# Kernel optimization log

Measured on AMD Instinct MI355X. Metric: run time of the kernel, lower is better.

The kernel has to match this reference:

```python
import jax, jax.numpy as jnp
import numpy as np

HIDDEN = 1024
BATCH = 8192
N_STEPS = 50


def setup_inputs() -> dict:
    key = jax.random.key(0)
    k1, k2, k3 = jax.random.split(key, 3)
    x0 = jax.random.normal(k1, (HIDDEN, BATCH), dtype=jnp.float32)
    W = jax.random.normal(k2, (HIDDEN, HIDDEN), dtype=jnp.float32) * (1.0 / np.sqrt(HIDDEN))
    b = jax.random.normal(k3, (HIDDEN, 1), dtype=jnp.float32)
    t0 = jnp.zeros((), dtype=jnp.float32)
    t1 = jnp.ones((), dtype=jnp.float32)
    return {"x0": x0, "t0": t0, "t1": t1, "W": W, "b": b}


def reference(x0, t0, t1, W, b):
    # Euler integration: x_{i+1} = x_i + h * (W @ x_i + b), h = (t1 - t0) / N
    h = (t1 - t0) / N_STEPS

    def step(x, _):
        x = x + h * (W @ x + b)  # b [H,1] broadcasts over batch
        return x, None

    x_final, _ = jax.lax.scan(step, x0, None, length=N_STEPS)
    return x_final
```

## Files before the change

### kernel.cpp

```cpp
#include <hip/hip_runtime.h>

#define H 1024
#define HH (H * H)
#define BATCH 8192
#define NSTEPS 50

typedef __attribute__((ext_vector_type(8))) short bf16x8;
typedef __attribute__((ext_vector_type(4))) float f32x4;

__device__ __forceinline__ void split2(float a, unsigned short& h, unsigned short& l)
{
    unsigned u = __float_as_uint(a);
    float r = a - __uint_as_float(u & 0xFFFF0000u);
    h = (unsigned short)(u >> 16);
    l = (unsigned short)((__float_as_uint(r) + 0x8000u) >> 16);
}
__device__ __forceinline__ unsigned short rnd_bf16(float a)
{
    return (unsigned short)((__float_as_uint(a) + 0x8000u) >> 16);
}
__device__ __forceinline__ float bf2f(unsigned short s)
{
    return __uint_as_float(((unsigned)s) << 16);
}
__device__ __forceinline__ void gload16(const void* g, void* l)
{
    __builtin_amdgcn_global_load_lds(
        (const __attribute__((address_space(1))) void*)g,
        (__attribute__((address_space(3))) void*)l, 16, 0, 0);
}
#define VMCNT(n) asm volatile("s_waitcnt vmcnt(" #n ")" ::: "memory")
#define RBAR() do { __builtin_amdgcn_s_barrier(); __builtin_amdgcn_sched_barrier(0); } while (0)

__global__ void setup_k(const float* __restrict__ W, const float* __restrict__ bvec,
                        const float* __restrict__ t0, const float* __restrict__ t1,
                        unsigned short* __restrict__ Aplanes,
                        float* __restrict__ cv, float* __restrict__ v0)
{
    __shared__ unsigned short th[64][68], tl[64][68];
    const float h = (t1[0] - t0[0]) / (float)NSTEPS;
    const int bid = blockIdx.x, tid = threadIdx.x;
    const int rb = (bid >> 4) * 64, cb = (bid & 15) * 64;
    const int row = tid >> 2, c16 = (tid & 3) * 16;

    unsigned short* Ahi  = Aplanes;
    unsigned short* Alo  = Aplanes + HH;
    unsigned short* AhiT = Aplanes + 2 * HH;
    unsigned short* AloT = Aplanes + 3 * HH;

    {
        const float* wsrc = &W[(size_t)(rb + row) * H + cb + c16];
        bf16x8 hv[2], lv[2];
        #pragma unroll
        for (int q = 0; q < 16; ++q) {
            const float a = h * wsrc[q] + ((rb + row) == (cb + c16 + q) ? 1.0f : 0.0f);
            unsigned short hh, ll;
            split2(a, hh, ll);
            hv[q >> 3][q & 7] = (short)hh;
            lv[q >> 3][q & 7] = (short)ll;
            th[row][c16 + q] = hh;
            tl[row][c16 + q] = ll;
        }
        *(bf16x8*)&Ahi[(size_t)(rb + row) * H + cb + c16] = hv[0];
        *(bf16x8*)&Ahi[(size_t)(rb + row) * H + cb + c16 + 8] = hv[1];
        *(bf16x8*)&Alo[(size_t)(rb + row) * H + cb + c16] = lv[0];
        *(bf16x8*)&Alo[(size_t)(rb + row) * H + cb + c16 + 8] = lv[1];
    }
    __syncthreads();
    {
        bf16x8 hv[2], lv[2];
        #pragma unroll
        for (int q = 0; q < 16; ++q) {
            hv[q >> 3][q & 7] = (short)th[c16 + q][row];
            lv[q >> 3][q & 7] = (short)tl[c16 + q][row];
        }
        *(bf16x8*)&AhiT[(size_t)(cb + row) * H + rb + c16] = hv[0];
        *(bf16x8*)&AhiT[(size_t)(cb + row) * H + rb + c16 + 8] = hv[1];
        *(bf16x8*)&AloT[(size_t)(cb + row) * H + rb + c16] = lv[0];
        *(bf16x8*)&AloT[(size_t)(cb + row) * H + rb + c16 + 8] = lv[1];
    }
    if (bid == 0) {
        #pragma unroll
        for (int rep = 0; rep < 4; ++rep) {
            const int i = tid + rep * 256;
            const float v = h * bvec[i];
            cv[i] = v; v0[i] = v;
        }
    }
}

template<bool WRITE_T, bool DO_X>
__launch_bounds__(512)
__global__ void chain_fused_k(const unsigned short* __restrict__ Lhi,
                              const unsigned short* __restrict__ Llo,
                              const unsigned short* __restrict__ RThi,
                              const unsigned short* __restrict__ RTlo,
                              unsigned short* __restrict__ Qhi,
                              unsigned short* __restrict__ Qlo,
                              unsigned short* __restrict__ QhiT,
                              unsigned short* __restrict__ QloT,
                              const float* __restrict__ vin,
                              const float* __restrict__ addv,
                              float* __restrict__ vout,
                              const float* __restrict__ X,
                              unsigned short* __restrict__ XhiT)
{
    __shared__ unsigned short sA[2][2][2][64][32];
    __shared__ unsigned short sB[2][2][2][64][32];

    const int tid = threadIdx.x;
    const int bid = blockIdx.x;
    const int wave = tid >> 6, lane = tid & 63;

    if (DO_X && bid >= 272) {
        float (*ts)[65] = (float(*)[65])&sA[0][0][0][0][0];
        const int tile = bid - 272;
        const int n0x = (tile >> 4) * 64, k0x = (tile & 15) * 64;
        #pragma unroll
        for (int p = 0; p < 2; ++p) {
            const int kr = p * 32 + (tid >> 4);
            const int c4 = (tid & 15) * 4;
            const float4 v = *(const float4*)&X[(size_t)(k0x + kr) * BATCH + n0x + c4];
            ts[kr][c4 + 0] = v.x; ts[kr][c4 + 1] = v.y;
            ts[kr][c4 + 2] = v.z; ts[kr][c4 + 3] = v.w;
        }
        __syncthreads();
        {
            const int n = tid >> 3;
            const int kc = (tid & 7) * 8;
            bf16x8 hv;
            #pragma unroll
            for (int q = 0; q < 8; ++q)
                hv[q] = (short)rnd_bf16(ts[kc + q][n]);
            *(bf16x8*)&XhiT[(size_t)(n0x + n) * H + k0x + kc] = hv;
        }
        return;
    }

    if (bid >= 256) {
        const int rowbase = (bid - 256) * 64 + wave * 8;
        const float4* xq = (const float4*)vin + lane * 4;
        float4 xv[4];
        #pragma unroll
        for (int q = 0; q < 4; ++q) xv[q] = xq[q];
        #pragma unroll
        for (int rr = 0; rr < 8; ++rr) {
            const int row = rowbase + rr;
            const unsigned short* mh = Lhi + (size_t)row * H + lane * 16;
            const unsigned short* ml = Llo + (size_t)row * H + lane * 16;
            bf16x8 h0 = *(const bf16x8*)&mh[0];
            bf16x8 h1 = *(const bf16x8*)&mh[8];
            bf16x8 l0 = *(const bf16x8*)&ml[0];
            bf16x8 l1 = *(const bf16x8*)&ml[8];
            float s = 0.0f;
            #pragma unroll
            for (int q = 0; q < 8; ++q) {
                const float m0v = bf2f((unsigned short)h0[q]) + bf2f((unsigned short)l0[q]);
                const float m1v = bf2f((unsigned short)h1[q]) + bf2f((unsigned short)l1[q]);
                const float* xf = (const float*)xv;
                s = fmaf(m0v, xf[q], s);
                s = fmaf(m1v, xf[8 + q], s);
            }
            #pragma unroll
            for (int off = 32; off; off >>= 1)
                s += __shfl_down(s, off, 64);
            if (lane == 0) vout[row] = addv[row] + s;
        }
        return;
    }

    const int lg = lane >> 4, lm = lane & 15;
    const int half = wave >> 2;
    const int wq = wave & 3;
    const int wr2 = (wq >> 1) * 32, wc2 = (wq & 1) * 32;
    const int xcd = bid & 7;
    const int idx0 = bid >> 3;
    const int mt = (xcd >> 1) * 4 + (idx0 & 3);
    const int nt = (xcd & 1) * 8 + (idx0 >> 2);
    const int m0 = mt * 64, n0 = nt * 64;

    f32x4 acc[2][2] = {};

    #define CSTAGE(tt, b) do {                                                   \
        _Pragma("unroll")                                                        \
        for (int it = 0; it < 4; ++it) {                                         \
            const int idx = tid + it * 512;                                      \
            const int mat = idx >> 10, kh = (idx >> 9) & 1;                      \
            const int plane = (idx >> 8) & 1;                                    \
            const int row = (idx >> 2) & 63, kc = idx & 3;                       \
            const int ks = kc ^ ((row >> 1) & 3);                                \
            const unsigned short* g = mat ? (plane ? RTlo : RThi)                \
                                          : (plane ? Llo : Lhi);                 \
            const int rb = mat ? n0 : m0;                                        \
            unsigned short* d = mat ? &sB[b][kh][plane][row][kc * 8]             \
                                    : &sA[b][kh][plane][row][kc * 8];            \
            gload16(g + (size_t)(rb + row) * H + kh * 512 + (tt) * 32 + ks * 8, d); \
        }                                                                        \
    } while (0)

    CSTAGE(0, 0);
    __syncthreads();
    int buf = 0;
    for (int t = 0; t < 16; ++t) {
        if (t + 1 < 16) CSTAGE(t + 1, buf ^ 1);
        bf16x8 ah[2], al[2], bh[2], bl[2];
        #pragma unroll
        for (int i = 0; i < 2; ++i) {
            const int row = wr2 + i * 16 + lm;
            const int sl = lg ^ ((row >> 1) & 3);
            ah[i] = *(const bf16x8*)&sA[buf][half][0][row][sl * 8];
            al[i] = *(const bf16x8*)&sA[buf][half][1][row][sl * 8];
            const int rn = wc2 + i * 16 + lm;
            const int sn = lg ^ ((rn >> 1) & 3);
            bh[i] = *(const bf16x8*)&sB[buf][half][0][rn][sn * 8];
            bl[i] = *(const bf16x8*)&sB[buf][half][1][rn][sn * 8];
        }
        #pragma unroll
        for (int i = 0; i < 2; ++i)
            #pragma unroll
            for (int j = 0; j < 2; ++j) {
                acc[i][j] = __builtin_amdgcn_mfma_f32_16x16x32_bf16(ah[i], bh[j], acc[i][j], 0, 0, 0);
                acc[i][j] = __builtin_amdgcn_mfma_f32_16x16x32_bf16(ah[i], bl[j], acc[i][j], 0, 0, 0);
                acc[i][j] = __builtin_amdgcn_mfma_f32_16x16x32_bf16(al[i], bh[j], acc[i][j], 0, 0, 0);
            }
        __syncthreads();
        buf ^= 1;
    }
    #undef CSTAGE

    float* red = (float*)&sA[0][0][0][0][0];
    const int ridx = wq * 64 + lane;
    if (half == 1) {
        float* dst = red + (size_t)ridx * 17;
        #pragma unroll
        for (int i = 0; i < 2; ++i)
            #pragma unroll
            for (int j = 0; j < 2; ++j)
                *(f32x4*)&dst[(i * 2 + j) * 4] = acc[i][j];
    }
    __syncthreads();
    if (half == 0) {
        const float* src = red + (size_t)ridx * 17;
        #pragma unroll
        for (int i = 0; i < 2; ++i)
            #pragma unroll
            for (int j = 0; j < 2; ++j) {
                const f32x4 p = *(const f32x4*)&src[(i * 2 + j) * 4];
                acc[i][j] += p;
            }
        #pragma unroll
        for (int i = 0; i < 2; ++i) {
            const int row0 = m0 + wr2 + i * 16 + lg * 4;
            #pragma unroll
            for (int j = 0; j < 2; ++j) {
                const int col = n0 + wc2 + j * 16 + lm;
                unsigned short hs[4], ls[4];
                #pragma unroll
                for (int r = 0; r < 4; ++r) {
                    split2(acc[i][j][r], hs[r], ls[r]);
                    Qhi[(size_t)(row0 + r) * H + col] = hs[r];
                    Qlo[(size_t)(row0 + r) * H + col] = ls[r];
                }
                if (WRITE_T) {
                    ushort4 th, tl;
                    th.x = hs[0]; th.y = hs[1]; th.z = hs[2]; th.w = hs[3];
                    tl.x = ls[0]; tl.y = ls[1]; tl.z = ls[2]; tl.w = ls[3];
                    *(ushort4*)&QhiT[(size_t)col * H + row0] = th;
                    *(ushort4*)&QloT[(size_t)col * H + row0] = tl;
                }
            }
        }
    }
}

__launch_bounds__(512)
__global__ void big_gemm_pipe_k(const unsigned short* __restrict__ Phi,
                                const unsigned short* __restrict__ Plo,
                                const unsigned short* __restrict__ XhiT,
                                float* __restrict__ C, const float* __restrict__ bias)
{
    __shared__ unsigned short sA[3][2][128][32];
    __shared__ unsigned short sB[3][256][32];

    const int tid = threadIdx.x;
    const int wave = tid >> 6, lane = tid & 63;
    const int lg = lane >> 4, lm = lane & 15;
    const int wr2 = (wave >> 2) * 64;
    const int wc2 = (wave & 3) * 64;
    const int bid = blockIdx.x;
    const int l = bid >> 3;
    const int m0 = (l & 7) * 128;
    const int n0 = ((bid & 7) * 4 + (l >> 3)) * 256;

    f32x4 acc[4][4] = {};

    #define BSTAGE(tt, b) do {                                                     \
        const int r_ = tid >> 2, kc_ = tid & 3;                                    \
        const int ks_ = kc_ ^ ((r_ >> 1) & 3);                                     \
        const size_t go_ = (size_t)(tt) * 32 + ks_ * 8;                            \
        gload16(Phi  + (size_t)(m0 + r_) * H + go_, &sA[b][0][r_][kc_ * 8]);       \
        gload16(Plo  + (size_t)(m0 + r_) * H + go_, &sA[b][1][r_][kc_ * 8]);       \
        gload16(XhiT + (size_t)(n0 + r_) * H + go_, &sB[b][r_][kc_ * 8]);          \
        gload16(XhiT + (size_t)(n0 + 128 + r_) * H + go_, &sB[b][128 + r_][kc_ * 8]); \
    } while (0)

    BSTAGE(0, 0);
    BSTAGE(1, 1);
    VMCNT(4);
    RBAR();

    #pragma unroll
    for (int t = 0; t < 32; ++t) {
        const int b = t % 3;
        bf16x8 ah[4], al[4], bh[4];
        #pragma unroll
        for (int i = 0; i < 4; ++i) {
            const int row = wr2 + i * 16 + lm;
            const int sl = lg ^ ((row >> 1) & 3);
            ah[i] = *(const bf16x8*)&sA[b][0][row][sl * 8];
            al[i] = *(const bf16x8*)&sA[b][1][row][sl * 8];
        }
        #pragma unroll
        for (int j = 0; j < 4; ++j) {
            const int rn = wc2 + j * 16 + lm;
            const int sn = lg ^ ((rn >> 1) & 3);
            bh[j] = *(const bf16x8*)&sB[b][rn][sn * 8];
        }
        if (t + 2 < 32) BSTAGE(t + 2, (t + 2) % 3);
        __builtin_amdgcn_s_setprio(1);
        #pragma unroll
        for (int i = 0; i < 4; ++i)
            #pragma unroll
            for (int j = 0; j < 4; ++j) {
                acc[i][j] = __builtin_amdgcn_mfma_f32_16x16x32_bf16(ah[i], bh[j], acc[i][j], 0, 0, 0);
                acc[i][j] = __builtin_amdgcn_mfma_f32_16x16x32_bf16(al[i], bh[j], acc[i][j], 0, 0, 0);
            }
        __builtin_amdgcn_s_setprio(0);
        if (t < 30) VMCNT(4);
        else if (t == 30) VMCNT(0);
        if (t < 31) RBAR();
    }
    #undef BSTAGE

    #pragma unroll
    for (int i = 0; i < 4; ++i) {
        const int row0 = m0 + wr2 + i * 16 + lg * 4;
        #pragma unroll
        for (int r = 0; r < 4; ++r) {
            const float bv = bias[row0 + r];
            float* dst = &C[(size_t)(row0 + r) * BATCH + n0 + wc2 + lm];
            #pragma unroll
            for (int j = 0; j < 4; ++j)
                dst[j * 16] = acc[i][j][r] + bv;
        }
    }
}

#define PADK 40

__launch_bounds__(256)
__global__ void big_gemm_k(const unsigned short* __restrict__ Ahi_g,
                           const unsigned short* __restrict__ Alo_g,
                           const float* __restrict__ X, float* __restrict__ C,
                           const float* __restrict__ bias)
{
    __shared__ unsigned short Ahi[128][PADK], Alo[128][PADK];
    __shared__ unsigned short Bhi[128][PADK], Blo[128][PADK];

    const int tid = threadIdx.x;
    const int wave = tid >> 6;
    const int lane = tid & 63;
    const int wr = (wave >> 1) * 64;
    const int wc = (wave & 1) * 64;
    const int m0 = blockIdx.y * 128;
    const int n0 = blockIdx.x * 128;
    const int lg = lane >> 4;
    const int lm = lane & 15;

    f32x4 acc[4][4] = {};

    for (int k0 = 0; k0 < H; k0 += 32) {
        #pragma unroll
        for (int a2 = 0; a2 < 2; ++a2) {
            const int id = tid + a2 * 256;
            const int row = id >> 2;
            const int ko = id & 3;
            const size_t g = (size_t)(m0 + row) * H + k0 + ko * 8;
            *(bf16x8*)&Ahi[row][ko * 8] = *(const bf16x8*)&Ahi_g[g];
            *(bf16x8*)&Alo[row][ko * 8] = *(const bf16x8*)&Alo_g[g];
        }
        #pragma unroll
        for (int a2 = 0; a2 < 2; ++a2) {
            const int id = tid + a2 * 256;
            const int n = id & 127;
            const int ko = id >> 7;
            const float* src = &X[(size_t)(k0 + ko * 8) * BATCH + n0 + n];
            bf16x8 bh, bl;
            #pragma unroll
            for (int i = 0; i < 8; ++i) {
                unsigned short hh, ll;
                split2(src[(size_t)i * BATCH], hh, ll);
                bh[i] = (short)hh;
                bl[i] = (short)ll;
            }
            *(bf16x8*)&Bhi[n][ko * 8] = bh;
            *(bf16x8*)&Blo[n][ko * 8] = bl;
        }
        __syncthreads();

        bf16x8 ah[4], al[4], bh[4], bl[4];
        #pragma unroll
        for (int i = 0; i < 4; ++i) {
            const int m = wr + i * 16 + lm;
            ah[i] = *(const bf16x8*)&Ahi[m][lg * 8];
            al[i] = *(const bf16x8*)&Alo[m][lg * 8];
            const int n = wc + i * 16 + lm;
            bh[i] = *(const bf16x8*)&Bhi[n][lg * 8];
            bl[i] = *(const bf16x8*)&Blo[n][lg * 8];
        }
        #pragma unroll
        for (int i = 0; i < 4; ++i)
            #pragma unroll
            for (int j = 0; j < 4; ++j) {
                acc[i][j] = __builtin_amdgcn_mfma_f32_16x16x32_bf16(ah[i], bh[j], acc[i][j], 0, 0, 0);
                acc[i][j] = __builtin_amdgcn_mfma_f32_16x16x32_bf16(ah[i], bl[j], acc[i][j], 0, 0, 0);
                acc[i][j] = __builtin_amdgcn_mfma_f32_16x16x32_bf16(al[i], bh[j], acc[i][j], 0, 0, 0);
            }
        __syncthreads();
    }

    #pragma unroll
    for (int i = 0; i < 4; ++i) {
        const int rowb = m0 + wr + i * 16 + lg * 4;
        #pragma unroll
        for (int r = 0; r < 4; ++r) {
            const float bv = bias[rowb + r];
            float* dst = &C[(size_t)(rowb + r) * BATCH + n0 + wc + lm];
            #pragma unroll
            for (int j = 0; j < 4; ++j)
                dst[j * 16] = acc[i][j][r] + bv;
        }
    }
}

extern "C" void kernel_launch(void* const* d_in, const int* in_sizes, int n_in,
                              void* d_out, int out_size, void* d_ws, size_t ws_size,
                              hipStream_t stream)
{
    const float* x0 = (const float*)d_in[0];
    const float* t0 = (const float*)d_in[1];
    const float* t1 = (const float*)d_in[2];
    const float* W  = (const float*)d_in[3];
    const float* bb = (const float*)d_in[4];
    float* out = (float*)d_out;

    unsigned short* Aplanes = (unsigned short*)d_ws;
    unsigned short* Ahi  = Aplanes;
    unsigned short* Alo  = Aplanes + HH;
    float* cv = (float*)(Aplanes + 4 * HH);
    float* v0 = cv + H;
    float* v1 = v0 + H;

    const size_t xtoff = (size_t)16 * 1024 * 1024;
    const bool useXT = ws_size >= xtoff + (size_t)BATCH * H * sizeof(unsigned short);
    unsigned short* XhiT = (unsigned short*)((char*)d_ws + xtoff);

    unsigned short* PA = (unsigned short*)d_out;
    unsigned short* PB = PA + (size_t)4 * HH;

    setup_k<<<256, 256, 0, stream>>>(W, bb, t0, t1, Aplanes, cv, v0);

    const int seq[7] = {0, 1, 0, 0, 0, 1, 0};
    unsigned short* cur = Ahi;
    float* vin = v0;
    float* vout = v1;
    for (int s = 0; s < 7; ++s) {
        const unsigned short* L  = seq[s] ? Ahi : cur;
        const unsigned short* Ll = seq[s] ? Alo : cur + HH;
        const float* addv = seq[s] ? cv : vin;
        if (s == 0) {
            unsigned short* nxt = PA;
            if (useXT) {
                chain_fused_k<true, true><<<2320, 512, 0, stream>>>(
                    L, Ll, cur + 2 * HH, cur + 3 * HH,
                    nxt, nxt + HH, nxt + 2 * HH, nxt + 3 * HH,
                    vin, addv, vout, x0, XhiT);
            } else {
                chain_fused_k<true, false><<<272, 512, 0, stream>>>(
                    L, Ll, cur + 2 * HH, cur + 3 * HH,
                    nxt, nxt + HH, nxt + 2 * HH, nxt + 3 * HH,
                    vin, addv, vout, nullptr, nullptr);
            }
            cur = nxt;
        } else if (s < 6) {
            unsigned short* nxt = (s & 1) ? PB : PA;
            chain_fused_k<true, false><<<272, 512, 0, stream>>>(
                L, Ll, cur + 2 * HH, cur + 3 * HH,
                nxt, nxt + HH, nxt + 2 * HH, nxt + 3 * HH,
                vin, addv, vout, nullptr, nullptr);
            cur = nxt;
        } else {
            chain_fused_k<false, false><<<272, 512, 0, stream>>>(
                L, Ll, cur + 2 * HH, cur + 3 * HH,
                Ahi, Alo, nullptr, nullptr,
                vin, addv, vout, nullptr, nullptr);
            cur = Ahi;
        }
        float* tv = vin; vin = vout; vout = tv;
    }

    if (useXT) {
        big_gemm_pipe_k<<<256, 512, 0, stream>>>(Ahi, Alo, XhiT, out, vin);
    } else {
        big_gemm_k<<<dim3(BATCH / 128, H / 128), 256, 0, stream>>>(
            Ahi, Alo, x0, out, vin);
    }
}
```

Baseline: 162.2 us.

## Use single bf16 plane for final propagator in big GEMM

The last chain step now writes only a rounded bf16 high plane (no lo plane or transposes), and the big output GEMM drops the lo-plane MFMA pass. This halves the MFMA work and A-operand traffic in the dominant GEMM. The GEMM is also reworked from a 3-stage, 512-thread, 128x256-tile pipeline to a 2-stage, 256-thread, 128x128-tile one with plain syncthreads. The cost is lower precision on the propagator matrix and a simpler pipeline that may hide load latency less well.

```diff
diff --git a/kernel.cpp b/kernel.cpp
--- a/kernel.cpp
+++ b/kernel.cpp
@@ -29,8 +29,6 @@
         (const __attribute__((address_space(1))) void*)g,
         (__attribute__((address_space(3))) void*)l, 16, 0, 0);
 }
-#define VMCNT(n) asm volatile("s_waitcnt vmcnt(" #n ")" ::: "memory")
-#define RBAR() do { __builtin_amdgcn_s_barrier(); __builtin_amdgcn_sched_barrier(0); } while (0)
 
 __global__ void setup_k(const float* __restrict__ W, const float* __restrict__ bvec,
                         const float* __restrict__ t0, const float* __restrict__ t1,
@@ -89,7 +87,7 @@
     }
 }
 
-template<bool WRITE_T, bool DO_X>
+template<bool WRITE_T, bool DO_X, bool PR>
 __launch_bounds__(512)
 __global__ void chain_fused_k(const unsigned short* __restrict__ Lhi,
                               const unsigned short* __restrict__ Llo,
@@ -254,91 +252,87 @@
             #pragma unroll
             for (int j = 0; j < 2; ++j) {
                 const int col = n0 + wc2 + j * 16 + lm;
-                unsigned short hs[4], ls[4];
-                #pragma unroll
-                for (int r = 0; r < 4; ++r) {
-                    split2(acc[i][j][r], hs[r], ls[r]);
-                    Qhi[(size_t)(row0 + r) * H + col] = hs[r];
-                    Qlo[(size_t)(row0 + r) * H + col] = ls[r];
+                if (PR) {
+                    #pragma unroll
+                    for (int r = 0; r < 4; ++r)
+                        Qhi[(size_t)(row0 + r) * H + col] = rnd_bf16(acc[i][j][r]);
+                } else {
+                    unsigned short hs[4], ls[4];
+                    #pragma unroll
+                    for (int r = 0; r < 4; ++r) {
+                        split2(acc[i][j][r], hs[r], ls[r]);
+                        Qhi[(size_t)(row0 + r) * H + col] = hs[r];
+                        Qlo[(size_t)(row0 + r) * H + col] = ls[r];
+                    }
+                    if (WRITE_T) {
+                        ushort4 th, tl;
+                        th.x = hs[0]; th.y = hs[1]; th.z = hs[2]; th.w = hs[3];
+                        tl.x = ls[0]; tl.y = ls[1]; tl.z = ls[2]; tl.w = ls[3];
+                        *(ushort4*)&QhiT[(size_t)col * H + row0] = th;
+                        *(ushort4*)&QloT[(size_t)col * H + row0] = tl;
+                    }
                 }
-                if (WRITE_T) {
-                    ushort4 th, tl;
-                    th.x = hs[0]; th.y = hs[1]; th.z = hs[2]; th.w = hs[3];
-                    tl.x = ls[0]; tl.y = ls[1]; tl.z = ls[2]; tl.w = ls[3];
-                    *(ushort4*)&QhiT[(size_t)col * H + row0] = th;
-                    *(ushort4*)&QloT[(size_t)col * H + row0] = tl;
-                }
-            }
-        }
-    }
-}
-
-__launch_bounds__(512)
-__global__ void big_gemm_pipe_k(const unsigned short* __restrict__ Phi,
-                                const unsigned short* __restrict__ Plo,
-                                const unsigned short* __restrict__ XhiT,
-                                float* __restrict__ C, const float* __restrict__ bias)
-{
-    __shared__ unsigned short sA[3][2][128][32];
-    __shared__ unsigned short sB[3][256][32];
+            }
+        }
+    }
+}
+
+__launch_bounds__(256)
+__global__ void big_gemm1_k(const unsigned short* __restrict__ Pr,
+                            const unsigned short* __restrict__ XhiT,
+                            float* __restrict__ C, const float* __restrict__ bias)
+{
+    __shared__ unsigned short sA[2][128][32];
+    __shared__ unsigned short sB[2][128][32];
 
     const int tid = threadIdx.x;
     const int wave = tid >> 6, lane = tid & 63;
     const int lg = lane >> 4, lm = lane & 15;
-    const int wr2 = (wave >> 2) * 64;
-    const int wc2 = (wave & 3) * 64;
+    const int wr2 = (wave >> 1) * 64;
+    const int wc2 = (wave & 1) * 64;
     const int bid = blockIdx.x;
     const int l = bid >> 3;
     const int m0 = (l & 7) * 128;
-    const int n0 = ((bid & 7) * 4 + (l >> 3)) * 256;
+    const int n0 = ((bid & 7) * 8 + (l >> 3)) * 128;
 
     f32x4 acc[4][4] = {};
 
-    #define BSTAGE(tt, b) do {                                                     \
-        const int r_ = tid >> 2, kc_ = tid & 3;                                    \
-        const int ks_ = kc_ ^ ((r_ >> 1) & 3);                                     \
-        const size_t go_ = (size_t)(tt) * 32 + ks_ * 8;                            \
-        gload16(Phi  + (size_t)(m0 + r_) * H + go_, &sA[b][0][r_][kc_ * 8]);       \
-        gload16(Plo  + (size_t)(m0 + r_) * H + go_, &sA[b][1][r_][kc_ * 8]);       \
-        gload16(XhiT + (size_t)(n0 + r_) * H + go_, &sB[b][r_][kc_ * 8]);          \
-        gload16(XhiT + (size_t)(n0 + 128 + r_) * H + go_, &sB[b][128 + r_][kc_ * 8]); \
+    #define BSTAGE(tt, b) do {                                                   \
+        _Pragma("unroll")                                                        \
+        for (int it = 0; it < 2; ++it) {                                         \
+            const int idx = tid + it * 256;                                      \
+            const int row = idx >> 2, kc = idx & 3;                              \
+            const int ks = kc ^ ((row >> 1) & 3);                                \
+            const size_t go = (size_t)(tt) * 32 + ks * 8;                        \
+            gload16(Pr   + (size_t)(m0 + row) * H + go, &sA[b][row][kc * 8]);    \
+            gload16(XhiT + (size_t)(n0 + row) * H + go, &sB[b][row][kc * 8]);    \
+        }                                                                        \
     } while (0)
 
     BSTAGE(0, 0);
-    BSTAGE(1, 1);
-    VMCNT(4);
-    RBAR();
-
-    #pragma unroll
+    __syncthreads();
+    int buf = 0;
     for (int t = 0; t < 32; ++t) {
-        const int b = t % 3;
-        bf16x8 ah[4], al[4], bh[4];
+        if (t + 1 < 32) BSTAGE(t + 1, buf ^ 1);
+        bf16x8 ah[4], bh[4];
         #pragma unroll
         for (int i = 0; i < 4; ++i) {
             const int row = wr2 + i * 16 + lm;
             const int sl = lg ^ ((row >> 1) & 3);
-            ah[i] = *(const bf16x8*)&sA[b][0][row][sl * 8];
-            al[i] = *(const bf16x8*)&sA[b][1][row][sl * 8];
-        }
-        #pragma unroll
-        for (int j = 0; j < 4; ++j) {
-            const int rn = wc2 + j * 16 + lm;
+            ah[i] = *(const bf16x8*)&sA[buf][row][sl * 8];
+            const int rn = wc2 + i * 16 + lm;
             const int sn = lg ^ ((rn >> 1) & 3);
-            bh[j] = *(const bf16x8*)&sB[b][rn][sn * 8];
-        }
-        if (t + 2 < 32) BSTAGE(t + 2, (t + 2) % 3);
+            bh[i] = *(const bf16x8*)&sB[buf][rn][sn * 8];
+        }
         __builtin_amdgcn_s_setprio(1);
         #pragma unroll
         for (int i = 0; i < 4; ++i)
             #pragma unroll
-            for (int j = 0; j < 4; ++j) {
+            for (int j = 0; j < 4; ++j)
                 acc[i][j] = __builtin_amdgcn_mfma_f32_16x16x32_bf16(ah[i], bh[j], acc[i][j], 0, 0, 0);
-                acc[i][j] = __builtin_amdgcn_mfma_f32_16x16x32_bf16(al[i], bh[j], acc[i][j], 0, 0, 0);
-            }
         __builtin_amdgcn_s_setprio(0);
-        if (t < 30) VMCNT(4);
-        else if (t == 30) VMCNT(0);
-        if (t < 31) RBAR();
+        __syncthreads();
+        buf ^= 1;
     }
     #undef BSTAGE
 
@@ -481,12 +475,12 @@
         if (s == 0) {
             unsigned short* nxt = PA;
             if (useXT) {
-                chain_fused_k<true, true><<<2320, 512, 0, stream>>>(
+                chain_fused_k<true, true, false><<<2320, 512, 0, stream>>>(
                     L, Ll, cur + 2 * HH, cur + 3 * HH,
                     nxt, nxt + HH, nxt + 2 * HH, nxt + 3 * HH,
                     vin, addv, vout, x0, XhiT);
             } else {
-                chain_fused_k<true, false><<<272, 512, 0, stream>>>(
+                chain_fused_k<true, false, false><<<272, 512, 0, stream>>>(
                     L, Ll, cur + 2 * HH, cur + 3 * HH,
                     nxt, nxt + HH, nxt + 2 * HH, nxt + 3 * HH,
                     vin, addv, vout, nullptr, nullptr);
@@ -494,13 +488,19 @@
             cur = nxt;
         } else if (s < 6) {
             unsigned short* nxt = (s & 1) ? PB : PA;
-            chain_fused_k<true, false><<<272, 512, 0, stream>>>(
+            chain_fused_k<true, false, false><<<272, 512, 0, stream>>>(
                 L, Ll, cur + 2 * HH, cur + 3 * HH,
                 nxt, nxt + HH, nxt + 2 * HH, nxt + 3 * HH,
                 vin, addv, vout, nullptr, nullptr);
             cur = nxt;
+        } else if (useXT) {
+            chain_fused_k<false, false, true><<<272, 512, 0, stream>>>(
+                L, Ll, cur + 2 * HH, cur + 3 * HH,
+                Ahi, nullptr, nullptr, nullptr,
+                vin, addv, vout, nullptr, nullptr);
+            cur = Ahi;
         } else {
-            chain_fused_k<false, false><<<272, 512, 0, stream>>>(
+            chain_fused_k<false, false, false><<<272, 512, 0, stream>>>(
                 L, Ll, cur + 2 * HH, cur + 3 * HH,
                 Ahi, Alo, nullptr, nullptr,
                 vin, addv, vout, nullptr, nullptr);
@@ -510,7 +510,7 @@
     }
 
     if (useXT) {
-        big_gemm_pipe_k<<<256, 512, 0, stream>>>(Ahi, Alo, XhiT, out, vin);
+        big_gemm1_k<<<512, 256, 0, stream>>>(Ahi, XhiT, out, vin);
     } else {
         big_gemm_k<<<dim3(BATCH / 128, H / 128), 256, 0, stream>>>(
             Ahi, Alo, x0, out, vin);
```

New measurement: 157.2 us. -3.1%, faster.
